# Performance work log

Hardware: AMD Instinct MI355X
Metric: run time of the kernel (lower is better)

## Reference

```python
import jax, jax.numpy as jnp
import numpy as np

N_NODES = 50000
N_EDGES = 800000
MUL = 16            # multiplicity of each irrep (16x0e + 16x1o)
RADIAL_IN = 8       # radial basis size
RADIAL_HID = 64
N_PATHS = 5         # TP paths: s*Y0->s, v.Yv->s, s*Yv->v, v*Y0->v, v x Yv->v
NUM_SPECIES = 4
AVG_NEIGH = 16.0


def setup_inputs() -> dict:
    key = jax.random.key(0)
    ks = jax.random.split(key, 16)
    inp = {
        'node_scalars': jax.random.normal(ks[0], (N_NODES, MUL), jnp.float32),
        'node_vectors': jax.random.normal(ks[1], (N_NODES, MUL * 3), jnp.float32),
        'edge_sh': jax.random.normal(ks[2], (N_EDGES, 4), jnp.float32),
        'radial_emb': jax.random.uniform(ks[3], (N_EDGES, RADIAL_IN), jnp.float32),
        'senders': jax.random.randint(ks[4], (N_EDGES,), 0, N_NODES, jnp.int32),
        'receivers': jax.random.randint(ks[5], (N_EDGES,), 0, N_NODES, jnp.int32),
        'species': jax.random.randint(ks[6], (N_NODES,), 0, NUM_SPECIES, jnp.int32),
        # learned params (fan-in scaled)
        'W_in_s': jax.random.normal(ks[7], (MUL, MUL), jnp.float32) / np.sqrt(MUL),
        'W_in_v': jax.random.normal(ks[8], (MUL, MUL), jnp.float32) / np.sqrt(MUL),
        'mlp_w1': jax.random.normal(ks[9], (RADIAL_IN, RADIAL_HID), jnp.float32) / np.sqrt(RADIAL_IN),
        'mlp_b1': jnp.zeros((RADIAL_HID,), jnp.float32),
        'mlp_w2': jax.random.normal(ks[10], (RADIAL_HID, N_PATHS * MUL), jnp.float32) / np.sqrt(RADIAL_HID),
        'W_out_s': jax.random.normal(ks[11], (2 * MUL, 2 * MUL), jnp.float32) / np.sqrt(2 * MUL),
        'W_out_v': jax.random.normal(ks[12], (3 * MUL, MUL), jnp.float32) / np.sqrt(3 * MUL),
        'sc_s': jax.random.normal(ks[13], (NUM_SPECIES, MUL, 2 * MUL), jnp.float32) / np.sqrt(MUL),
        'sc_v': jax.random.normal(ks[14], (NUM_SPECIES, MUL, MUL), jnp.float32) / np.sqrt(MUL),
    }
    return inp


def reference(node_scalars, node_vectors, edge_sh, radial_emb, senders, receivers,
              species, W_in_s, W_in_v, mlp_w1, mlp_b1, mlp_w2, W_out_s, W_out_v,
              sc_s, sc_v):
    N = node_scalars.shape[0]
    inv_sqrt_deg = 1.0 / np.sqrt(AVG_NEIGH)

    # ---- input per-irrep linear ----
    s = node_scalars @ W_in_s                                  # [N,16]
    v_in = node_vectors.reshape(N, MUL, 3)
    v = jnp.einsum('nuc,uw->nwc', v_in, W_in_v)                # [N,16,3]

    # ---- gather sender features ----
    xs = s[senders]                                            # [E,16]
    xv = v[senders]                                            # [E,16,3]
    Y0 = edge_sh[:, :1]                                        # [E,1] l=0 SH
    Yv = edge_sh[:, 1:4]                                       # [E,3] l=1 SH

    # ---- radial MLP -> per-path tensor-product weights ----
    h = jax.nn.silu(radial_emb @ mlp_w1 + mlp_b1)              # [E,64]
    w = (h @ mlp_w2).reshape(-1, N_PATHS, MUL)                 # [E,5,16]

    # ---- CG tensor product (uvu) messages ----
    m_s1 = w[:, 0] * xs * Y0                                   # 0e x 0e -> 0e
    m_s2 = w[:, 1] * jnp.einsum('euc,ec->eu', xv, Yv)          # 1o x 1o -> 0e (dot)
    m_v1 = w[:, 2, :, None] * xs[:, :, None] * Yv[:, None, :]  # 0e x 1o -> 1o
    m_v2 = w[:, 3, :, None] * xv * Y0[:, :, None]              # 1o x 0e -> 1o
    m_v3 = w[:, 4, :, None] * jnp.cross(xv, Yv[:, None, :])    # 1o x 1o -> 1o (cross)

    # ---- scatter-sum to receivers + neighbour normalization ----
    m_s = jnp.concatenate([m_s1, m_s2], axis=-1)               # [E,32]
    m_v = jnp.concatenate([m_v1, m_v2, m_v3], axis=1)          # [E,48,3]
    a_s = jax.ops.segment_sum(m_s, receivers, num_segments=N) * inv_sqrt_deg
    a_v = jax.ops.segment_sum(m_v, receivers, num_segments=N) * inv_sqrt_deg

    # ---- output per-irrep linear ----
    pre_s = a_s @ W_out_s                                      # [N,32]
    pre_v = jnp.einsum('nuc,uw->nwc', a_v, W_out_v)            # [N,16,3]

    # ---- species-dependent self connection ----
    pre_s = pre_s + jnp.einsum('nu,nuw->nw', node_scalars, sc_s[species])
    pre_v = pre_v + jnp.einsum('nuc,nuw->nwc', v_in, sc_v[species])

    # ---- gate nonlinearity ----
    out_s = jax.nn.silu(pre_s[:, :MUL])                        # scalar outputs
    gates = jax.nn.sigmoid(pre_s[:, MUL:])                     # gate scalars
    out_v = pre_v * gates[:, :, None]

    # ---- resnet ----
    out_s = out_s + node_scalars
    out_v = out_v + v_in

    return jnp.concatenate([out_s, out_v.reshape(N, MUL * 3)], axis=-1)
```

## Files before the change

kernel.cpp:

```cpp
#include <hip/hip_runtime.h>
#include <hip/hip_bf16.h>

typedef unsigned short u16;
typedef unsigned int   u32;
typedef _Float16 h2 __attribute__((ext_vector_type(2)));
typedef short s8v __attribute__((ext_vector_type(8)));
typedef float f4v __attribute__((ext_vector_type(4)));
typedef u16 u16x4 __attribute__((ext_vector_type(4)));

#define N_NODES 50000
#define N_EDGES 800000
#define NCH   2
#define RPC   25000
#define CHMAX 409600

#define RPB   250
#define NBINS 200
#define EPB   4096
#define NBB   ((N_EDGES+EPB-1)/EPB)

#define WB_W1H  0
#define WB_B1   256
#define WB_W2F  320
#define WB_WINS 2880
#define WB_WINV 3136
#define WB_WOS  3392
#define WB_WOV  4416
#define WB_SCS  5184
#define WB_SCV  7232
#define WB_FLAG 8256
#define OFF_SV16 8260
#define IDX_BCNT 1608260
#define IDX_BOF2 1608516
#define IDX_BCUR 1608772
#define IDX_OFFS 1658260
#define IDX_BUCK 1758262
#define IDX_EEID 2558264
#define OFF_ER16 3358264
#define OFF_WPA  3758264
#define OFF_WPB  16865464
#define OFF_YB   20142264
#define OFF_SND  21780664
#define OFF_REC  21985472
#define ACC_OFF  34785472

__device__ __forceinline__ float bf2f(u16 v){
  union { u32 u; float f; } x; x.u = ((u32)v) << 16; return x.f;
}
__device__ __forceinline__ u16 f2bf(float f){
  u32 u = __float_as_uint(f);
  u32 lsb = (u >> 16) & 1u;
  u32 r = u + 0x7fffu + lsb;
  return (u16)(r >> 16);
}
__device__ __forceinline__ float ldx(const void* p, long long i, int isf){
  return isf ? ((const float*)p)[i] : bf2f(((const u16*)p)[i]);
}
__device__ __forceinline__ u32 pkh2(float a, float b){
  union { u32 u; h2 v; } x; x.v.x = (_Float16)a; x.v.y = (_Float16)b; return x.u;
}
__device__ __forceinline__ float dot2(h2 a, u32 w, float c){
  union { u32 u; h2 v; } x; x.u = w;
#if __has_builtin(__builtin_amdgcn_fdot2)
  return __builtin_amdgcn_fdot2(a, x.v, c, false);
#else
  return c + (float)a.x*(float)x.v.x + (float)a.y*(float)x.v.y;
#endif
}
__device__ __forceinline__ float sigmoidf_(float x){ return 1.f/(1.f + __expf(-x)); }

__global__ void detect_dtype(const u32* __restrict__ remb_raw, int* __restrict__ flag){
  int t = threadIdx.x;
  u32 w = remb_raw[t];
  u32 lo = w & 0xffffu, hi = w >> 16;
  int okl = ((lo & 0x8000u) == 0) && (((lo >> 7) & 0xffu) <= 126u);
  int okh = ((hi & 0x8000u) == 0) && (((hi >> 7) & 0xffu) <= 126u);
  unsigned long long bad = __ballot(!(okl && okh));
  if (t == 0) *flag = (bad != 0ull) ? 1 : 0;
}

__global__ void prep_weights(const void* __restrict__ w1, const void* __restrict__ b1g,
                             const void* __restrict__ w2, const void* __restrict__ wins,
                             const void* __restrict__ winv, const void* __restrict__ wos,
                             const void* __restrict__ wov, const void* __restrict__ scs,
                             const void* __restrict__ scv, float* __restrict__ wbuf,
                             const int* __restrict__ flag){
  int t = threadIdx.x;
  int isf = *flag;
  u32* w1h  = (u32*)(wbuf + WB_W1H);
  u16* w2f  = (u16*)(wbuf + WB_W2F);
  for (int idx=t; idx<256;  idx+=256){
    int j = idx>>2, ip = idx&3;
    w1h[idx] = pkh2(ldx(w1, (2*ip)*64+j, isf), ldx(w1, (2*ip+1)*64+j, isf));
  }
  for (int idx=t; idx<64;   idx+=256){ wbuf[WB_B1+idx]  = ldx(b1g, idx, isf); }
  for (int idx=t; idx<5120; idx+=256){
    int tt = idx >> 10;
    int rem = idx & 1023;
    int kh = rem >> 9;
    int rem2 = rem & 511;
    int ln = rem2 >> 3, j = rem2 & 7;
    int k = kh*32 + (ln>>4)*8 + j;
    int o = tt*16 + (ln&15);
    w2f[idx] = f2bf(ldx(w2, (long long)k*80 + o, isf));
  }
  for (int idx=t; idx<256;  idx+=256){ wbuf[WB_WINS+idx] = ldx(wins, idx, isf); }
  for (int idx=t; idx<256;  idx+=256){ wbuf[WB_WINV+idx] = ldx(winv, idx, isf); }
  for (int idx=t; idx<1024; idx+=256){ wbuf[WB_WOS+idx]  = ldx(wos, idx, isf); }
  for (int idx=t; idx<768;  idx+=256){ wbuf[WB_WOV+idx]  = ldx(wov, idx, isf); }
  for (int idx=t; idx<2048; idx+=256){ wbuf[WB_SCS+idx]  = ldx(scs, idx, isf); }
  for (int idx=t; idx<1024; idx+=256){ wbuf[WB_SCV+idx]  = ldx(scv, idx, isf); }
}

__global__ void __launch_bounds__(256) node_pre(
    const void* __restrict__ ns_g, const void* __restrict__ nv_g,
    const float* __restrict__ wbuf, u16* __restrict__ sv16,
    const int* __restrict__ flag){
  __shared__ float A[16][16];
  __shared__ float B[16][48];
  __shared__ float wsl[256], wvl[256];
  int tid = threadIdx.x;
  int isf = *flag;
  int n0 = blockIdx.x*16;
  for (int i=tid;i<256;i+=256){ wsl[i]=wbuf[WB_WINS+i]; wvl[i]=wbuf[WB_WINV+i]; }
  for (int i=tid;i<256;i+=256) A[i>>4][i&15] = ldx(ns_g,(long long)n0*16+i,isf);
  for (int i=tid;i<768;i+=256) B[i/48][i%48] = ldx(nv_g,(long long)n0*48+i,isf);
  __syncthreads();
  int g = tid>>4, u = tid&15;
  float s=0.f, v0=0.f, v1=0.f, v2=0.f;
  #pragma unroll
  for (int j=0;j<16;j++){
    s  += A[g][j]*wsl[j*16+u];
    float wv = wvl[j*16+u];
    v0 += B[g][j*3+0]*wv;
    v1 += B[g][j*3+1]*wv;
    v2 += B[g][j*3+2]*wv;
  }
  u16x4 pk;
  pk[0]=f2bf(s); pk[1]=f2bf(v0); pk[2]=f2bf(v1); pk[3]=f2bf(v2);
  ((u16x4*)sv16)[(size_t)(n0+g)*16 + u] = pk;
}

__global__ void __launch_bounds__(256) pack_edges(
    const void* __restrict__ remb, const void* __restrict__ edge_sh,
    const int* __restrict__ senders, u32* __restrict__ rec,
    const int* __restrict__ flag){
  int e = blockIdx.x*256 + threadIdx.x;
  if (e >= N_EDGES) return;
  int isf = *flag;
  if (isf){
    u32* r = rec + (size_t)e*16;
    f4v ra = ((const f4v*)remb)[(size_t)e*2];
    f4v rb = ((const f4v*)remb)[(size_t)e*2+1];
    ((f4v*)r)[0] = ra;
    ((f4v*)r)[1] = rb;
    ((f4v*)r)[2] = ((const f4v*)edge_sh)[e];
    r[12] = (u32)senders[e];
  } else {
    u32* r = rec + (size_t)e*8;
    *(s8v*)r = ((const s8v*)remb)[e];
    const u32* ys = (const u32*)edge_sh + (size_t)e*2;
    r[4]=ys[0]; r[5]=ys[1];
    r[6] = (u32)senders[e];
    r[7] = 0;
  }
}

__global__ void __launch_bounds__(256) bin_count(const int* __restrict__ receivers,
                                                 int* __restrict__ bcnt){
  __shared__ int lcnt[NBINS];
  int t = threadIdx.x;
  for (int i=t;i<NBINS;i+=256) lcnt[i]=0;
  __syncthreads();
  int base = blockIdx.x*EPB;
  for (int i=t;i<EPB;i+=256){
    int e = base+i;
    if (e<N_EDGES) atomicAdd(&lcnt[receivers[e]/RPB],1);
  }
  __syncthreads();
  for (int i=t;i<NBINS;i+=256) if (lcnt[i]) atomicAdd(&bcnt[i], lcnt[i]);
}

__global__ void bin_scan(const int* __restrict__ bcnt, int* __restrict__ binoff,
                         int* __restrict__ bincur, int* __restrict__ offs){
  __shared__ int lds[NBINS];
  int t=threadIdx.x;
  if (t<NBINS) lds[t]=bcnt[t];
  __syncthreads();
  for (int off=1; off<NBINS; off<<=1){
    int v = (t<NBINS && t>=off)? lds[t-off] : 0;
    __syncthreads();
    if (t<NBINS) lds[t]+=v;
    __syncthreads();
  }
  if (t<NBINS){ int ex = lds[t]-bcnt[t]; binoff[t]=ex; bincur[t]=ex; }
  if (t==0) offs[N_NODES] = N_EDGES;
}

__global__ void __launch_bounds__(256) bin_scatter(const int* __restrict__ receivers,
                 int* __restrict__ bincur, u32* __restrict__ eeid, u16* __restrict__ er){
  __shared__ int lcnt[NBINS], loff[NBINS], lcur[NBINS], gbase[NBINS];
  __shared__ u32 seid[EPB];
  __shared__ u16 sr[EPB];
  int t = threadIdx.x;
  for (int i=t;i<NBINS;i+=256) lcnt[i]=0;
  __syncthreads();
  int base = blockIdx.x*EPB;
  int r_[16];
  #pragma unroll
  for (int k=0;k<16;k++){
    int e = base + t + k*256;
    r_[k] = (e<N_EDGES)? receivers[e] : -1;
    if (r_[k]>=0) atomicAdd(&lcnt[r_[k]/RPB],1);
  }
  __syncthreads();
  if (t<NBINS) loff[t]=lcnt[t];
  __syncthreads();
  for (int off=1; off<NBINS; off<<=1){
    int v=(t<NBINS&&t>=off)?loff[t-off]:0;
    __syncthreads();
    if (t<NBINS) loff[t]+=v;
    __syncthreads();
  }
  if (t<NBINS){
    int ex=loff[t]-lcnt[t]; loff[t]=ex; lcur[t]=ex;
    gbase[t] = lcnt[t] ? atomicAdd(&bincur[t], lcnt[t]) : 0;
  }
  __syncthreads();
  #pragma unroll
  for (int k=0;k<16;k++){
    if (r_[k]>=0){
      int b=r_[k]/RPB;
      int p=atomicAdd(&lcur[b],1);
      seid[p]=(u32)(base + t + k*256);
      sr[p]=(u16)r_[k];
    }
  }
  __syncthreads();
  int rem = N_EDGES - base;
  int tot = rem < EPB ? rem : EPB;
  for (int i=t;i<tot;i+=256){
    int b = sr[i]/RPB;
    int dst = gbase[b] + (i - loff[b]);
    eeid[dst]=seid[i]; er[dst]=sr[i];
  }
}

__global__ void __launch_bounds__(256) bin_finalize(const u32* __restrict__ eeid,
        const u16* __restrict__ er, const int* __restrict__ binoff,
        const int* __restrict__ bcnt, int* __restrict__ offs, int* __restrict__ bucket){
  __shared__ int deg[RPB], pfx[RPB], lcur[RPB];
  int b=blockIdx.x, t=threadIdx.x;
  int beg=binoff[b], cnt=bcnt[b];
  for (int i=t;i<RPB;i+=256) deg[i]=0;
  __syncthreads();
  int r0=b*RPB;
  for (int i=t;i<cnt;i+=256) atomicAdd(&deg[er[beg+i]-r0],1);
  __syncthreads();
  if (t<RPB) pfx[t]=deg[t];
  __syncthreads();
  for (int off=1; off<RPB; off<<=1){
    int v=(t<RPB&&t>=off)?pfx[t-off]:0;
    __syncthreads();
    if (t<RPB) pfx[t]+=v;
    __syncthreads();
  }
  if (t<RPB){
    int ex=pfx[t]-deg[t]; pfx[t]=ex; lcur[t]=ex;
    offs[r0+t]=beg+ex;
  }
  __syncthreads();
  for (int i=t;i<cnt;i+=256){
    int rr = er[beg+i]-r0;
    int k = atomicAdd(&lcur[rr],1);
    bucket[beg+k] = (int)eeid[beg+i];
  }
}

__global__ void __launch_bounds__(256) pass1_w(
    const int* __restrict__ bucket, const int* __restrict__ offs,
    const u32* __restrict__ rec, const float* __restrict__ wbuf,
    u16* __restrict__ wpA, u16* __restrict__ wpB,
    float* __restrict__ ybf, u16* __restrict__ snd16,
    int rlo, const int* __restrict__ flag){
  __shared__ u16 hlds[4*16*72];
  int tid = threadIdx.x;
  int lane = tid & 63, wid = tid >> 6;
  int isf = *flag;
  int chunkBeg = offs[rlo], chunkEnd = offs[rlo + RPC];
  int r0e = chunkBeg + (blockIdx.x*4 + wid)*16;
  if (r0e >= chunkEnd) return;
  u16* hw = hlds + wid*(16*72);
  int e = lane & 15, q = lane >> 4;

  int er = r0e + e;
  int eid = (er < chunkEnd) ? bucket[er] : 0;
  float re[8];
  if (isf){
    const u32* r = rec + (size_t)eid*16;
    f4v ra = ((const f4v*)r)[0];
    f4v rb = ((const f4v*)r)[1];
    re[0]=ra[0]; re[1]=ra[1]; re[2]=ra[2]; re[3]=ra[3];
    re[4]=rb[0]; re[5]=rb[1]; re[6]=rb[2]; re[7]=rb[3];
    if (q == 0 && er < chunkEnd){
      size_t widx = (size_t)(er - chunkBeg);
      ((f4v*)ybf)[widx] = ((const f4v*)r)[2];
      snd16[widx] = (u16)r[12];
    }
  } else {
    const u32* r = rec + (size_t)eid*8;
    s8v r8 = *(const s8v*)r;
    #pragma unroll
    for (int i=0;i<8;i++) re[i] = bf2f((u16)r8[i]);
    if (q == 0 && er < chunkEnd){
      size_t widx = (size_t)(er - chunkBeg);
      u32 y0 = r[4], y1 = r[5];
      f4v y;
      y[0]=bf2f((u16)(y0 & 0xffffu)); y[1]=bf2f((u16)(y0 >> 16));
      y[2]=bf2f((u16)(y1 & 0xffffu)); y[3]=bf2f((u16)(y1 >> 16));
      ((f4v*)ybf)[widx] = y;
      snd16[widx] = (u16)r[6];
    }
  }
  h2 reh[4];
  #pragma unroll
  for (int ip=0;ip<4;ip++){ reh[ip].x=(_Float16)re[2*ip]; reh[ip].y=(_Float16)re[2*ip+1]; }
  const u32* w1h = (const u32*)(wbuf + WB_W1H);
  const float* b1 = wbuf + WB_B1;
  #pragma unroll
  for (int jj=0;jj<16;jj++){
    int j = q*16 + jj;
    float a = b1[j];
    #pragma unroll
    for (int ip=0;ip<4;ip++) a = dot2(reh[ip], w1h[j*4+ip], a);
    a = a * sigmoidf_(a);
    hw[e*72 + j] = f2bf(a);
  }
  asm volatile("s_waitcnt lgkmcnt(0)" ::: "memory");

  const u16* w2f = (const u16*)(wbuf + WB_W2F);
  s8v bfr[5][2];
  #pragma unroll
  for (int t=0;t<5;t++)
    #pragma unroll
    for (int kh=0;kh<2;kh++)
      bfr[t][kh] = *(const s8v*)(w2f + ((t*2+kh)*64 + lane)*8);

  f4v acc[5];
  #pragma unroll
  for (int t=0;t<5;t++) acc[t] = (f4v){0.f,0.f,0.f,0.f};
  #pragma unroll
  for (int kh=0;kh<2;kh++){
    s8v af = *(const s8v*)(hw + e*72 + kh*32 + q*8);
    #pragma unroll
    for (int t=0;t<5;t++)
      acc[t] = __builtin_amdgcn_mfma_f32_16x16x32_bf16(af, bfr[t][kh], acc[t], 0,0,0);
  }
  int n = lane & 15;
  #pragma unroll
  for (int r=0;r<4;r++){
    int er2 = r0e + q*4 + r;
    if (er2 < chunkEnd){
      size_t widx = (size_t)(er2 - chunkBeg);
      u16x4 pk4;
      pk4[0]=f2bf(acc[0][r]); pk4[1]=f2bf(acc[1][r]);
      pk4[2]=f2bf(acc[2][r]); pk4[3]=f2bf(acc[3][r]);
      ((u16x4*)wpA)[widx*16 + n] = pk4;
      wpB[widx*16 + n] = f2bf(acc[4][r]);
    }
  }
}

__global__ void __launch_bounds__(256, 4) pass2_reduce(
    const int* __restrict__ offs,
    const u16* __restrict__ sv16, const u16* __restrict__ wpA,
    const u16* __restrict__ wpB, const float* __restrict__ ybf,
    const u16* __restrict__ snd16, float* __restrict__ accbuf,
    int rlo){
  __shared__ float part[4][176];
  int tid = threadIdx.x;
  int lane = tid & 63, wid = tid >> 6;
  int u = lane & 15, q = lane >> 4;
  int pr = wid >> 1;
  int wsub = wid & 1;
  int r = rlo + blockIdx.x*2 + pr;
  int chunkBeg = offs[rlo];
  int beg = offs[r], end = offs[r+1];
  float As0=0.f,As1=0.f;
  float Av00=0.f,Av01=0.f,Av02=0.f, Av10=0.f,Av11=0.f,Av12=0.f, Av20=0.f,Av21=0.f,Av22=0.f;
  auto body = [&](int rank){
    size_t li = (size_t)(rank - chunkBeg);
    f4v y = ((const f4v*)ybf)[li];
    float Y0=y[0], Yv0=y[1], Yv1=y[2], Yv2=y[3];
    int snd = snd16[li];
    u16x4 wv = ((const u16x4*)wpA)[li*16 + u];
    float w0=bf2f(wv[0]), w1=bf2f(wv[1]), w2=bf2f(wv[2]), w3=bf2f(wv[3]);
    float w4=bf2f(wpB[li*16 + u]);
    u16x4 sv = *(const u16x4*)(sv16 + ((size_t)snd*16 + u)*4);
    float xs=bf2f(sv[0]), x0=bf2f(sv[1]), x1=bf2f(sv[2]), x2=bf2f(sv[3]);
    As0 += w0*xs*Y0;
    As1 += w1*(x0*Yv0 + x1*Yv1 + x2*Yv2);
    float t1 = w2*xs;  Av00 += t1*Yv0; Av01 += t1*Yv1; Av02 += t1*Yv2;
    float t2 = w3*Y0;  Av10 += t2*x0;  Av11 += t2*x1;  Av12 += t2*x2;
    Av20 += w4*(x1*Yv2 - x2*Yv1);
    Av21 += w4*(x2*Yv0 - x0*Yv2);
    Av22 += w4*(x0*Yv1 - x1*Yv0);
  };
  int rank = beg + wsub*4 + q;
  for (; rank + 8 < end; rank += 16){ body(rank); body(rank+8); }
  if (rank < end) body(rank);
  #define RED2(x) { x += __shfl_xor(x,16); x += __shfl_xor(x,32); }
  RED2(As0) RED2(As1)
  RED2(Av00) RED2(Av01) RED2(Av02)
  RED2(Av10) RED2(Av11) RED2(Av12)
  RED2(Av20) RED2(Av21) RED2(Av22)
  #undef RED2
  if (q == 0){
    float* pp = part[wid];
    pp[u]=As0;      pp[16+u]=As1;
    pp[32+u]=Av00;  pp[48+u]=Av10;  pp[64+u]=Av20;
    pp[80+u]=Av01;  pp[96+u]=Av11;  pp[112+u]=Av21;
    pp[128+u]=Av02; pp[144+u]=Av12; pp[160+u]=Av22;
  }
  __syncthreads();
  for (int i = tid; i < 352; i += 256){
    int pr2 = i / 176, idx = i - pr2*176;
    int rr = blockIdx.x*2 + pr2;
    accbuf[(size_t)rr*176 + idx] = part[pr2*2][idx] + part[pr2*2+1][idx];
  }
}

__global__ void __launch_bounds__(256) pass2_epilogue(
    const float* __restrict__ accbuf, const float* __restrict__ wbuf,
    const void* __restrict__ ns_g, const void* __restrict__ nv_g,
    const int* __restrict__ species, void* __restrict__ out,
    int rlo, const int* __restrict__ flag){
  __shared__ float sb[16*176 + 16*16 + 16*48];
  int tid = threadIdx.x;
  int isf = *flag;
  int n0 = rlo + blockIdx.x*16;
  int rem = rlo + RPC - n0;
  int nblk = rem < 16 ? rem : 16;
  {
    int tot = nblk*176;
    const float* src = accbuf + (size_t)(n0 - rlo)*176;
    for (int i=tid; i<tot; i+=256) sb[i] = src[i];
    float* nsb = sb + 2816;
    for (int i=tid; i<nblk*16; i+=256)
      nsb[i] = ldx(ns_g, (long long)n0*16 + i, isf);
    float* vinb = sb + 2816 + 256;
    for (int i=tid; i<nblk*48; i+=256)
      vinb[i] = ldx(nv_g, (long long)n0*48 + i, isf);
  }
  __syncthreads();
  int g = tid >> 4, u = tid & 15;
  if (g >= nblk) return;
  int nn = n0 + g;
  const float* bin  = sb + g*176;
  const float* nsb  = sb + 2816 + g*16;
  const float* vinb = sb + 2816 + 256 + g*48;
  int sp = species[nn];
  const float* wos = wbuf + WB_WOS;
  const float* scs = wbuf + WB_SCS + sp*512;
  const float* wov = wbuf + WB_WOV;
  const float* scv = wbuf + WB_SCV + sp*256;
  float p0 = 0.f, p1 = 0.f;
  #pragma unroll
  for (int j=0;j<32;j++){
    float a = bin[j]*0.25f;
    p0 += a*wos[j*32+u];
    p1 += a*wos[j*32+16+u];
  }
  #pragma unroll
  for (int j=0;j<16;j++){
    float nu = nsb[j];
    p0 += nu*scs[j*32+u];
    p1 += nu*scs[j*32+16+u];
  }
  float gate = sigmoidf_(p1);
  float os = p0*sigmoidf_(p0) + nsb[u];
  float pv0, pv1, pv2;
  {
    float a0=0.f, a1=0.f, a2=0.f;
    #pragma unroll
    for (int j=0;j<48;j++){
      float wv = wov[j*16+u];
      a0 += bin[32 + 0*48 + j]*0.25f*wv;
      a1 += bin[32 + 1*48 + j]*0.25f*wv;
      a2 += bin[32 + 2*48 + j]*0.25f*wv;
    }
    #pragma unroll
    for (int j=0;j<16;j++){
      float sv = scv[j*16+u];
      a0 += vinb[j*3+0]*sv;
      a1 += vinb[j*3+1]*sv;
      a2 += vinb[j*3+2]*sv;
    }
    pv0 = a0*gate + vinb[u*3+0];
    pv1 = a1*gate + vinb[u*3+1];
    pv2 = a2*gate + vinb[u*3+2];
  }
  if (isf){
    float* orow = (float*)out + (size_t)nn*64;
    orow[u] = os;
    orow[16 + u*3 + 0] = pv0;
    orow[16 + u*3 + 1] = pv1;
    orow[16 + u*3 + 2] = pv2;
  } else {
    u16* orow = (u16*)out + (size_t)nn*64;
    orow[u] = f2bf(os);
    orow[16 + u*3 + 0] = f2bf(pv0);
    orow[16 + u*3 + 1] = f2bf(pv1);
    orow[16 + u*3 + 2] = f2bf(pv2);
  }
}

extern "C" void kernel_launch(void* const* d_in, const int* in_sizes, int n_in,
                              void* d_out, int out_size, void* d_ws, size_t ws_size,
                              hipStream_t stream){
  const void* node_scalars = d_in[0];
  const void* node_vectors = d_in[1];
  const void* edge_sh      = d_in[2];
  const void* radial_emb   = d_in[3];
  const int* senders      = (const int*)d_in[4];
  const int* receivers    = (const int*)d_in[5];
  const int* species      = (const int*)d_in[6];
  const void* W_in_s  = d_in[7];
  const void* W_in_v  = d_in[8];
  const void* mlp_w1  = d_in[9];
  const void* mlp_b1  = d_in[10];
  const void* mlp_w2  = d_in[11];
  const void* W_out_s = d_in[12];
  const void* W_out_v = d_in[13];
  const void* sc_s    = d_in[14];
  const void* sc_v    = d_in[15];

  float* wsf  = (float*)d_ws;
  int*   wsi  = (int*)d_ws;
  u32*   wsu  = (u32*)d_ws;
  float* wbuf = wsf;
  u16*   sv16 = (u16*)(wsu + OFF_SV16);
  int*   bcnt = wsi + IDX_BCNT;
  int*   bof2 = wsi + IDX_BOF2;
  int*   bcur = wsi + IDX_BCUR;
  int*   offs = wsi + IDX_OFFS;
  int*   buck = wsi + IDX_BUCK;
  u32*   eeid = wsu + IDX_EEID;
  u16*   er16 = (u16*)(wsu + OFF_ER16);
  u16*   wpA  = (u16*)(wsu + OFF_WPA);
  u16*   wpB  = (u16*)(wsu + OFF_WPB);
  float* ybf  = wsf + OFF_YB;
  u16*   snd16= (u16*)(wsu + OFF_SND);
  u32*   rec  = wsu + OFF_REC;
  float* accb = wsf + ACC_OFF;
  int*   flag = (int*)(wbuf + WB_FLAG);

  detect_dtype<<<1,64,0,stream>>>((const u32*)radial_emb, flag);
  hipMemsetAsync(bcnt, 0, NBINS*sizeof(int), stream);
  prep_weights<<<1,256,0,stream>>>(mlp_w1, mlp_b1, mlp_w2, W_in_s, W_in_v,
                                   W_out_s, W_out_v, sc_s, sc_v, wbuf, flag);
  node_pre<<<N_NODES/16,256,0,stream>>>(node_scalars, node_vectors, wbuf,
                                        sv16, flag);
  pack_edges<<<(N_EDGES+255)/256,256,0,stream>>>(radial_emb, edge_sh, senders,
                                                 rec, flag);
  bin_count<<<NBB,256,0,stream>>>(receivers, bcnt);
  bin_scan<<<1,256,0,stream>>>(bcnt, bof2, bcur, offs);
  bin_scatter<<<NBB,256,0,stream>>>(receivers, bcur, eeid, er16);
  bin_finalize<<<NBINS,256,0,stream>>>(eeid, er16, bof2, bcnt, offs, buck);
  for (int c = 0; c < NCH; c++){
    int rlo = c * RPC;
    pass1_w<<<CHMAX/64, 256, 0, stream>>>(buck, offs, rec, wbuf,
                                          wpA, wpB, ybf, snd16, rlo, flag);
    pass2_reduce<<<RPC/2, 256, 0, stream>>>(offs, sv16, wpA, wpB, ybf, snd16,
                                            accb, rlo);
    pass2_epilogue<<<(RPC+15)/16, 256, 0, stream>>>(accb, wbuf, node_scalars,
                                                    node_vectors, species,
                                                    d_out, rlo, flag);
  }
}
```

Measured before the change: 386.0 us.

## Fuse radial MLP weight computation into per-receiver reduction via LDS staging

```diff
diff --git a/kernel.cpp b/kernel.cpp
--- a/kernel.cpp
+++ b/kernel.cpp
@@ -10,14 +10,13 @@
 
 #define N_NODES 50000
 #define N_EDGES 800000
-#define NCH   2
-#define RPC   25000
-#define CHMAX 409600
 
 #define RPB   250
 #define NBINS 200
 #define EPB   4096
 #define NBB   ((N_EDGES+EPB-1)/EPB)
+
+#define EPS   64
 
 #define WB_W1H  0
 #define WB_B1   256
@@ -37,12 +36,8 @@
 #define IDX_BUCK 1758262
 #define IDX_EEID 2558264
 #define OFF_ER16 3358264
-#define OFF_WPA  3758264
-#define OFF_WPB  16865464
-#define OFF_YB   20142264
-#define OFF_SND  21780664
-#define OFF_REC  21985472
-#define ACC_OFF  34785472
+#define OFF_REC  3758264
+#define ACC_OFF  16558264
 
 __device__ __forceinline__ float bf2f(u16 v){
   union { u32 u; float f; } x; x.u = ((u32)v) << 16; return x.f;
@@ -277,67 +272,29 @@
   }
 }
 
-__global__ void __launch_bounds__(256) pass1_w(
+__global__ void __launch_bounds__(256, 4) pass_fused(
     const int* __restrict__ bucket, const int* __restrict__ offs,
     const u32* __restrict__ rec, const float* __restrict__ wbuf,
-    u16* __restrict__ wpA, u16* __restrict__ wpB,
-    float* __restrict__ ybf, u16* __restrict__ snd16,
-    int rlo, const int* __restrict__ flag){
-  __shared__ u16 hlds[4*16*72];
+    const u16* __restrict__ sv16, float* __restrict__ accbuf,
+    const int* __restrict__ flag){
+  __shared__ u16  wp[5][EPS][16];
+  __shared__ float yb[EPS][4];
+  __shared__ u16  sn[EPS];
+  __shared__ u16  hlds[4*16*72];
+  __shared__ float part[4][176];
   int tid = threadIdx.x;
   int lane = tid & 63, wid = tid >> 6;
+  int u = lane & 15, q = lane >> 4;
   int isf = *flag;
-  int chunkBeg = offs[rlo], chunkEnd = offs[rlo + RPC];
-  int r0e = chunkBeg + (blockIdx.x*4 + wid)*16;
-  if (r0e >= chunkEnd) return;
-  u16* hw = hlds + wid*(16*72);
-  int e = lane & 15, q = lane >> 4;
-
-  int er = r0e + e;
-  int eid = (er < chunkEnd) ? bucket[er] : 0;
-  float re[8];
-  if (isf){
-    const u32* r = rec + (size_t)eid*16;
-    f4v ra = ((const f4v*)r)[0];
-    f4v rb = ((const f4v*)r)[1];
-    re[0]=ra[0]; re[1]=ra[1]; re[2]=ra[2]; re[3]=ra[3];
-    re[4]=rb[0]; re[5]=rb[1]; re[6]=rb[2]; re[7]=rb[3];
-    if (q == 0 && er < chunkEnd){
-      size_t widx = (size_t)(er - chunkBeg);
-      ((f4v*)ybf)[widx] = ((const f4v*)r)[2];
-      snd16[widx] = (u16)r[12];
-    }
-  } else {
-    const u32* r = rec + (size_t)eid*8;
-    s8v r8 = *(const s8v*)r;
-    #pragma unroll
-    for (int i=0;i<8;i++) re[i] = bf2f((u16)r8[i]);
-    if (q == 0 && er < chunkEnd){
-      size_t widx = (size_t)(er - chunkBeg);
-      u32 y0 = r[4], y1 = r[5];
-      f4v y;
-      y[0]=bf2f((u16)(y0 & 0xffffu)); y[1]=bf2f((u16)(y0 >> 16));
-      y[2]=bf2f((u16)(y1 & 0xffffu)); y[3]=bf2f((u16)(y1 >> 16));
-      ((f4v*)ybf)[widx] = y;
-      snd16[widx] = (u16)r[6];
-    }
-  }
-  h2 reh[4];
-  #pragma unroll
-  for (int ip=0;ip<4;ip++){ reh[ip].x=(_Float16)re[2*ip]; reh[ip].y=(_Float16)re[2*ip+1]; }
+  int r0n = blockIdx.x*2;
+  int beg = offs[r0n], end = offs[r0n+2];
+  int cnt = end - beg;
+  int nsweep = (cnt + EPS - 1) / EPS;
+  int pr = wid >> 1, wsub = wid & 1;
+  int rbeg = offs[r0n + pr], rend = offs[r0n + pr + 1];
+
   const u32* w1h = (const u32*)(wbuf + WB_W1H);
   const float* b1 = wbuf + WB_B1;
-  #pragma unroll
-  for (int jj=0;jj<16;jj++){
-    int j = q*16 + jj;
-    float a = b1[j];
-    #pragma unroll
-    for (int ip=0;ip<4;ip++) a = dot2(reh[ip], w1h[j*4+ip], a);
-    a = a * sigmoidf_(a);
-    hw[e*72 + j] = f2bf(a);
-  }
-  asm volatile("s_waitcnt lgkmcnt(0)" ::: "memory");
-
   const u16* w2f = (const u16*)(wbuf + WB_W2F);
   s8v bfr[5][2];
   #pragma unroll
@@ -345,70 +302,106 @@
     #pragma unroll
     for (int kh=0;kh<2;kh++)
       bfr[t][kh] = *(const s8v*)(w2f + ((t*2+kh)*64 + lane)*8);
-
-  f4v acc[5];
-  #pragma unroll
-  for (int t=0;t<5;t++) acc[t] = (f4v){0.f,0.f,0.f,0.f};
-  #pragma unroll
-  for (int kh=0;kh<2;kh++){
-    s8v af = *(const s8v*)(hw + e*72 + kh*32 + q*8);
-    #pragma unroll
-    for (int t=0;t<5;t++)
-      acc[t] = __builtin_amdgcn_mfma_f32_16x16x32_bf16(af, bfr[t][kh], acc[t], 0,0,0);
-  }
-  int n = lane & 15;
-  #pragma unroll
-  for (int r=0;r<4;r++){
-    int er2 = r0e + q*4 + r;
-    if (er2 < chunkEnd){
-      size_t widx = (size_t)(er2 - chunkBeg);
-      u16x4 pk4;
-      pk4[0]=f2bf(acc[0][r]); pk4[1]=f2bf(acc[1][r]);
-      pk4[2]=f2bf(acc[2][r]); pk4[3]=f2bf(acc[3][r]);
-      ((u16x4*)wpA)[widx*16 + n] = pk4;
-      wpB[widx*16 + n] = f2bf(acc[4][r]);
-    }
-  }
-}
-
-__global__ void __launch_bounds__(256, 4) pass2_reduce(
-    const int* __restrict__ offs,
-    const u16* __restrict__ sv16, const u16* __restrict__ wpA,
-    const u16* __restrict__ wpB, const float* __restrict__ ybf,
-    const u16* __restrict__ snd16, float* __restrict__ accbuf,
-    int rlo){
-  __shared__ float part[4][176];
-  int tid = threadIdx.x;
-  int lane = tid & 63, wid = tid >> 6;
-  int u = lane & 15, q = lane >> 4;
-  int pr = wid >> 1;
-  int wsub = wid & 1;
-  int r = rlo + blockIdx.x*2 + pr;
-  int chunkBeg = offs[rlo];
-  int beg = offs[r], end = offs[r+1];
+  u16* hw = hlds + wid*(16*72);
+
   float As0=0.f,As1=0.f;
   float Av00=0.f,Av01=0.f,Av02=0.f, Av10=0.f,Av11=0.f,Av12=0.f, Av20=0.f,Av21=0.f,Av22=0.f;
-  auto body = [&](int rank){
-    size_t li = (size_t)(rank - chunkBeg);
-    f4v y = ((const f4v*)ybf)[li];
-    float Y0=y[0], Yv0=y[1], Yv1=y[2], Yv2=y[3];
-    int snd = snd16[li];
-    u16x4 wv = ((const u16x4*)wpA)[li*16 + u];
-    float w0=bf2f(wv[0]), w1=bf2f(wv[1]), w2=bf2f(wv[2]), w3=bf2f(wv[3]);
-    float w4=bf2f(wpB[li*16 + u]);
-    u16x4 sv = *(const u16x4*)(sv16 + ((size_t)snd*16 + u)*4);
-    float xs=bf2f(sv[0]), x0=bf2f(sv[1]), x1=bf2f(sv[2]), x2=bf2f(sv[3]);
-    As0 += w0*xs*Y0;
-    As1 += w1*(x0*Yv0 + x1*Yv1 + x2*Yv2);
-    float t1 = w2*xs;  Av00 += t1*Yv0; Av01 += t1*Yv1; Av02 += t1*Yv2;
-    float t2 = w3*Y0;  Av10 += t2*x0;  Av11 += t2*x1;  Av12 += t2*x2;
-    Av20 += w4*(x1*Yv2 - x2*Yv1);
-    Av21 += w4*(x2*Yv0 - x0*Yv2);
-    Av22 += w4*(x0*Yv1 - x1*Yv0);
-  };
-  int rank = beg + wsub*4 + q;
-  for (; rank + 8 < end; rank += 16){ body(rank); body(rank+8); }
-  if (rank < end) body(rank);
+
+  for (int s=0; s<nsweep; s++){
+    int sbeg = beg + s*EPS;
+    int tbase = sbeg + wid*16;
+    if (tbase < end){
+      int e = lane & 15;
+      int er = tbase + e;
+      int eid = (er < end) ? bucket[er] : 0;
+      float re[8];
+      if (isf){
+        const u32* r = rec + (size_t)eid*16;
+        f4v ra = ((const f4v*)r)[0];
+        f4v rb = ((const f4v*)r)[1];
+        re[0]=ra[0]; re[1]=ra[1]; re[2]=ra[2]; re[3]=ra[3];
+        re[4]=rb[0]; re[5]=rb[1]; re[6]=rb[2]; re[7]=rb[3];
+        if (q == 0 && er < end){
+          int le = er - sbeg;
+          *(f4v*)yb[le] = ((const f4v*)r)[2];
+          sn[le] = (u16)r[12];
+        }
+      } else {
+        const u32* r = rec + (size_t)eid*8;
+        s8v r8 = *(const s8v*)r;
+        #pragma unroll
+        for (int i=0;i<8;i++) re[i] = bf2f((u16)r8[i]);
+        if (q == 0 && er < end){
+          int le = er - sbeg;
+          u32 y0 = r[4], y1 = r[5];
+          f4v y;
+          y[0]=bf2f((u16)(y0 & 0xffffu)); y[1]=bf2f((u16)(y0 >> 16));
+          y[2]=bf2f((u16)(y1 & 0xffffu)); y[3]=bf2f((u16)(y1 >> 16));
+          *(f4v*)yb[le] = y;
+          sn[le] = (u16)r[6];
+        }
+      }
+      h2 reh[4];
+      #pragma unroll
+      for (int ip=0;ip<4;ip++){ reh[ip].x=(_Float16)re[2*ip]; reh[ip].y=(_Float16)re[2*ip+1]; }
+      asm volatile("s_waitcnt lgkmcnt(0)" ::: "memory");
+      #pragma unroll
+      for (int jj=0;jj<16;jj++){
+        int j = q*16 + jj;
+        float a = b1[j];
+        #pragma unroll
+        for (int ip=0;ip<4;ip++) a = dot2(reh[ip], w1h[j*4+ip], a);
+        a = a * sigmoidf_(a);
+        hw[e*72 + j] = f2bf(a);
+      }
+      asm volatile("s_waitcnt lgkmcnt(0)" ::: "memory");
+      f4v acc[5];
+      #pragma unroll
+      for (int t=0;t<5;t++) acc[t] = (f4v){0.f,0.f,0.f,0.f};
+      #pragma unroll
+      for (int kh=0;kh<2;kh++){
+        s8v af = *(const s8v*)(hw + e*72 + kh*32 + q*8);
+        #pragma unroll
+        for (int t=0;t<5;t++)
+          acc[t] = __builtin_amdgcn_mfma_f32_16x16x32_bf16(af, bfr[t][kh], acc[t], 0,0,0);
+      }
+      #pragma unroll
+      for (int r=0;r<4;r++){
+        int er2 = tbase + q*4 + r;
+        if (er2 < end){
+          int le = er2 - sbeg;
+          #pragma unroll
+          for (int t=0;t<5;t++) wp[t][le][u] = f2bf(acc[t][r]);
+        }
+      }
+    }
+    __syncthreads();
+    int lo = rbeg > sbeg ? rbeg : sbeg;
+    int hi = rend < sbeg + EPS ? rend : sbeg + EPS;
+    if (lo < hi){
+      int c = wsub*4 + q;
+      int off0 = (lo - rbeg) & 7;
+      int st = (c - off0) & 7;
+      for (int rank = lo + st; rank < hi; rank += 8){
+        int li = rank - sbeg;
+        f4v y = *(const f4v*)yb[li];
+        float Y0=y[0], Yv0=y[1], Yv1=y[2], Yv2=y[3];
+        int snd = sn[li];
+        float w0=bf2f(wp[0][li][u]), w1=bf2f(wp[1][li][u]), w2=bf2f(wp[2][li][u]);
+        float w3=bf2f(wp[3][li][u]), w4=bf2f(wp[4][li][u]);
+        u16x4 sv = *(const u16x4*)(sv16 + ((size_t)snd*16 + u)*4);
+        float xs=bf2f(sv[0]), x0=bf2f(sv[1]), x1=bf2f(sv[2]), x2=bf2f(sv[3]);
+        As0 += w0*xs*Y0;
+        As1 += w1*(x0*Yv0 + x1*Yv1 + x2*Yv2);
+        float t1 = w2*xs;  Av00 += t1*Yv0; Av01 += t1*Yv1; Av02 += t1*Yv2;
+        float t2 = w3*Y0;  Av10 += t2*x0;  Av11 += t2*x1;  Av12 += t2*x2;
+        Av20 += w4*(x1*Yv2 - x2*Yv1);
+        Av21 += w4*(x2*Yv0 - x0*Yv2);
+        Av22 += w4*(x0*Yv1 - x1*Yv0);
+      }
+    }
+    __syncthreads();
+  }
   #define RED2(x) { x += __shfl_xor(x,16); x += __shfl_xor(x,32); }
   RED2(As0) RED2(As1)
   RED2(Av00) RED2(Av01) RED2(Av02)
@@ -425,8 +418,7 @@
   __syncthreads();
   for (int i = tid; i < 352; i += 256){
     int pr2 = i / 176, idx = i - pr2*176;
-    int rr = blockIdx.x*2 + pr2;
-    accbuf[(size_t)rr*176 + idx] = part[pr2*2][idx] + part[pr2*2+1][idx];
+    accbuf[(size_t)(r0n + pr2)*176 + idx] = part[pr2*2][idx] + part[pr2*2+1][idx];
   }
 }
 
@@ -434,16 +426,16 @@
     const float* __restrict__ accbuf, const float* __restrict__ wbuf,
     const void* __restrict__ ns_g, const void* __restrict__ nv_g,
     const int* __restrict__ species, void* __restrict__ out,
-    int rlo, const int* __restrict__ flag){
+    const int* __restrict__ flag){
   __shared__ float sb[16*176 + 16*16 + 16*48];
   int tid = threadIdx.x;
   int isf = *flag;
-  int n0 = rlo + blockIdx.x*16;
-  int rem = rlo + RPC - n0;
+  int n0 = blockIdx.x*16;
+  int rem = N_NODES - n0;
   int nblk = rem < 16 ? rem : 16;
   {
     int tot = nblk*176;
-    const float* src = accbuf + (size_t)(n0 - rlo)*176;
+    const float* src = accbuf + (size_t)n0*176;
     for (int i=tid; i<tot; i+=256) sb[i] = src[i];
     float* nsb = sb + 2816;
     for (int i=tid; i<nblk*16; i+=256)
@@ -547,10 +539,6 @@
   int*   buck = wsi + IDX_BUCK;
   u32*   eeid = wsu + IDX_EEID;
   u16*   er16 = (u16*)(wsu + OFF_ER16);
-  u16*   wpA  = (u16*)(wsu + OFF_WPA);
-  u16*   wpB  = (u16*)(wsu + OFF_WPB);
-  float* ybf  = wsf + OFF_YB;
-  u16*   snd16= (u16*)(wsu + OFF_SND);
   u32*   rec  = wsu + OFF_REC;
   float* accb = wsf + ACC_OFF;
   int*   flag = (int*)(wbuf + WB_FLAG);
@@ -567,14 +555,8 @@
   bin_scan<<<1,256,0,stream>>>(bcnt, bof2, bcur, offs);
   bin_scatter<<<NBB,256,0,stream>>>(receivers, bcur, eeid, er16);
   bin_finalize<<<NBINS,256,0,stream>>>(eeid, er16, bof2, bcnt, offs, buck);
-  for (int c = 0; c < NCH; c++){
-    int rlo = c * RPC;
-    pass1_w<<<CHMAX/64, 256, 0, stream>>>(buck, offs, rec, wbuf,
-                                          wpA, wpB, ybf, snd16, rlo, flag);
-    pass2_reduce<<<RPC/2, 256, 0, stream>>>(offs, sv16, wpA, wpB, ybf, snd16,
-                                            accb, rlo);
-    pass2_epilogue<<<(RPC+15)/16, 256, 0, stream>>>(accb, wbuf, node_scalars,
-                                                    node_vectors, species,
-                                                    d_out, rlo, flag);
-  }
-}
+  pass_fused<<<N_NODES/2,256,0,stream>>>(buck, offs, rec, wbuf, sv16, accb, flag);
+  pass2_epilogue<<<(N_NODES+15)/16,256,0,stream>>>(accb, wbuf, node_scalars,
+                                                   node_vectors, species,
+                                                   d_out, flag);
+}
```

Result: slower. 469.3 us (+21.6%).
